# Optimization experiments

Hardware: AMD Instinct MI355X
Metric: run time of the kernel (lower is better)

## Reference

```python
import jax, jax.numpy as jnp
import numpy as np

DIM = 1024
HEADS = 16
HEAD_DIM = DIM // HEADS
SCALE = DIM ** (-0.5)  # note: module scales by full dim, not head_dim


def setup_inputs() -> dict:
    key = jax.random.key(0)
    k1, k2, k3, k4 = jax.random.split(key, 4)
    B, N = 4, 2048
    x = jax.random.normal(k1, (B, N, DIM), dtype=jnp.float32)
    # nn.Linear(dim, 3*dim, bias=False): weight [3*dim, dim]
    w_qkv = jax.random.normal(k2, (3 * DIM, DIM), dtype=jnp.float32) * (DIM ** -0.5)
    # nn.Linear(dim, dim) with bias
    w_out = jax.random.normal(k3, (DIM, DIM), dtype=jnp.float32) * (DIM ** -0.5)
    b_out = jax.random.normal(k4, (DIM,), dtype=jnp.float32) * 0.01
    return {"x": x, "w_qkv": w_qkv, "w_out": w_out, "b_out": b_out}


def reference(x, w_qkv, w_out, b_out):
    b, n, _ = x.shape
    qkv = jnp.einsum('bnd,ed->bne', x, w_qkv)  # [b, n, 3*dim]
    # rearrange 'b n (qkv h d) -> qkv b h n d'
    qkv = qkv.reshape(b, n, 3, HEADS, HEAD_DIM)
    q, k, v = (qkv[:, :, i].transpose(0, 2, 1, 3) for i in range(3))  # [b, h, n, d]
    dots = jnp.einsum('bhid,bhjd->bhij', q, k) * SCALE
    attn = jax.nn.softmax(dots, axis=-1)
    out = jnp.einsum('bhij,bhjd->bhid', attn, v)
    out = out.transpose(0, 2, 1, 3).reshape(b, n, HEADS * HEAD_DIM)  # [b, n, dim]
    return jnp.einsum('bnd,ed->bne', out, w_out) + b_out
```

## Files before the change

### kernel.cpp

```cpp
#include <hip/hip_runtime.h>

typedef __bf16 bf16_t;
typedef __bf16 bf16x2 __attribute__((ext_vector_type(2)));
typedef __bf16 bf16x4 __attribute__((ext_vector_type(4)));
typedef __bf16 bf16x8 __attribute__((ext_vector_type(8)));
typedef float floatx4 __attribute__((ext_vector_type(4)));

__device__ __forceinline__ void gll16(const void* g, void* l) {
  __builtin_amdgcn_global_load_lds(
      (const __attribute__((address_space(1))) void*)g,
      (__attribute__((address_space(3))) void*)l, 16, 0, 0);
}

__device__ __forceinline__ bf16x8 cvt8(const float4 a, const float4 b) {
  bf16x8 v;
  v[0] = (bf16_t)a.x; v[1] = (bf16_t)a.y; v[2] = (bf16_t)a.z; v[3] = (bf16_t)a.w;
  v[4] = (bf16_t)b.x; v[5] = (bf16_t)b.y; v[6] = (bf16_t)b.z; v[7] = (bf16_t)b.w;
  return v;
}

__global__ __launch_bounds__(256)
void cvt_f32_bf16(const float* __restrict__ src, bf16_t* __restrict__ dst, int n8)
{
  const int i = blockIdx.x * 256 + threadIdx.x;
  if (i < n8) {
    const float4 a = ((const float4*)src)[2 * i];
    const float4 b = ((const float4*)src)[2 * i + 1];
    *(bf16x8*)(dst + (size_t)i * 8) = cvt8(a, b);
  }
}

template<bool A32, bool W32, bool C32>
__global__ __launch_bounds__(256, 2)
void gemm_bt(const void* __restrict__ Av, const void* __restrict__ Wv,
             const float* __restrict__ bias, void* __restrict__ Cv,
             int M, int Nf, int K, int lda)
{
  __shared__ __align__(16) bf16_t lA[128 * 32];
  __shared__ __align__(16) bf16_t lB[128 * 32];

  const int tid  = threadIdx.x;
  const int wave = tid >> 6;
  const int lane = tid & 63;
  const int q    = lane >> 4;
  const int ln   = lane & 15;
  const int wm   = wave >> 1, wn = wave & 1;

  const int mtiles = M >> 7;
  const int mt = blockIdx.x % mtiles;
  const int nt = blockIdx.x / mtiles;
  const int m0 = mt << 7, n0 = nt << 7;

  floatx4 acc[4][4] = {};

  for (int k0 = 0; k0 < K; k0 += 32) {
    if constexpr (A32) {
      const float* Af = (const float*)Av;
#pragma unroll
      for (int sub = 0; sub < 2; ++sub) {
        const int r  = sub * 64 + (tid >> 2);
        const int c8 = tid & 3;
        const float* s = Af + (size_t)(m0 + r) * lda + k0 + c8 * 8;
        const float4 f0 = *(const float4*)s;
        const float4 f1 = *(const float4*)(s + 4);
        *(bf16x8*)(lA + r * 32 + (c8 ^ ((r >> 1) & 3)) * 8) = cvt8(f0, f1);
      }
    } else {
      const bf16_t* Ab = (const bf16_t*)Av;
#pragma unroll
      for (int half = 0; half < 2; ++half) {
        const int rbase = half * 64 + wave * 16;
        const int r  = rbase + (lane >> 2);
        const int gc = (lane & 3) ^ ((r >> 1) & 3);
        gll16(Ab + (size_t)(m0 + r) * lda + k0 + gc * 8, lA + rbase * 32);
      }
    }
    if constexpr (W32) {
      const float* Wf = (const float*)Wv;
#pragma unroll
      for (int sub = 0; sub < 2; ++sub) {
        const int r  = sub * 64 + (tid >> 2);
        const int c8 = tid & 3;
        const float* s = Wf + (size_t)(n0 + r) * K + k0 + c8 * 8;
        const float4 f0 = *(const float4*)s;
        const float4 f1 = *(const float4*)(s + 4);
        *(bf16x8*)(lB + r * 32 + (c8 ^ ((r >> 1) & 3)) * 8) = cvt8(f0, f1);
      }
    } else {
      const bf16_t* Wb = (const bf16_t*)Wv;
#pragma unroll
      for (int half = 0; half < 2; ++half) {
        const int rbase = half * 64 + wave * 16;
        const int r  = rbase + (lane >> 2);
        const int gc = (lane & 3) ^ ((r >> 1) & 3);
        gll16(Wb + (size_t)(n0 + r) * K + k0 + gc * 8, lB + rbase * 32);
      }
    }
    __syncthreads();

    bf16x8 af[4], bfr[4];
#pragma unroll
    for (int i = 0; i < 4; ++i) {
      const int r = wm * 64 + i * 16 + ln;
      af[i] = *(const bf16x8*)(lA + r * 32 + (q ^ ((r >> 1) & 3)) * 8);
    }
#pragma unroll
    for (int j = 0; j < 4; ++j) {
      const int r = wn * 64 + j * 16 + ln;
      bfr[j] = *(const bf16x8*)(lB + r * 32 + (q ^ ((r >> 1) & 3)) * 8);
    }
#pragma unroll
    for (int i = 0; i < 4; ++i)
#pragma unroll
      for (int j = 0; j < 4; ++j)
        acc[i][j] = __builtin_amdgcn_mfma_f32_16x16x32_bf16(af[i], bfr[j], acc[i][j], 0, 0, 0);
    __syncthreads();
  }

#pragma unroll
  for (int j = 0; j < 4; ++j) {
    const int col = n0 + wn * 64 + j * 16 + ln;
    const float bv = bias ? bias[col] : 0.0f;
#pragma unroll
    for (int i = 0; i < 4; ++i) {
      const int row = m0 + wm * 64 + i * 16 + q * 4;
#pragma unroll
      for (int r = 0; r < 4; ++r) {
        const float val = acc[i][j][r] + bv;
        if constexpr (C32)
          ((float*)Cv)[(size_t)(row + r) * Nf + col] = val;
        else
          ((bf16_t*)Cv)[(size_t)(row + r) * Nf + col] = (bf16_t)val;
      }
    }
  }
}

__global__ __launch_bounds__(256, 2)
void attn_kernel(bf16_t* __restrict__ qkv)
{
  __shared__ __align__(16) bf16_t lK[128 * 64];
  __shared__ __align__(16) bf16_t lV[128 * 66];
  __shared__ __align__(16) bf16_t lP[128 * 132];

  const int tid  = threadIdx.x;
  const int wave = tid >> 6;
  const int lane = tid & 63;
  const int q  = lane >> 4;
  const int ln = lane & 15;
  const int wm = wave >> 1, wn = wave & 1;

  const int bx = blockIdx.x;
  const int qt = bx & 15;
  const int h  = (bx >> 4) & 15;
  const int b  = bx >> 8;

  bf16_t* Qbase = qkv + (size_t)(b * 2048 + qt * 128) * 3072 + h * 64;
  const bf16_t* Kbase = qkv + (size_t)(b * 2048) * 3072 + 1024 + h * 64;
  const bf16_t* Vbase = qkv + (size_t)(b * 2048) * 3072 + 2048 + h * 64;

#pragma unroll
  for (int t = 0; t < 4; ++t) {
    const int rbase = t * 32 + wave * 8;
    const int r  = rbase + (lane >> 3);
    const int gc = (lane & 7) ^ (r & 7);
    gll16(Qbase + (size_t)r * 3072 + gc * 8, lP + rbase * 64);
  }
  __syncthreads();

  bf16x8 qf[4][2];
#pragma unroll
  for (int i = 0; i < 4; ++i) {
    const int r = wm * 64 + i * 16 + ln;
#pragma unroll
    for (int kt = 0; kt < 2; ++kt) {
      const int c = (kt * 4 + q) ^ (r & 7);
      qf[i][kt] = *(const bf16x8*)(lP + r * 64 + c * 8);
    }
  }
  __syncthreads();

  floatx4 accO[4][2] = {};
  floatx4 accS[4] = {};

  bf16x8 ones;
#pragma unroll
  for (int j = 0; j < 8; ++j) ones[j] = (bf16_t)1.0f;

  for (int jt = 0; jt < 16; ++jt) {
    const int j0 = jt * 128;

#pragma unroll
    for (int t = 0; t < 4; ++t) {
      const int rbase = t * 32 + wave * 8;
      const int r  = rbase + (lane >> 3);
      const int gc = (lane & 7) ^ (r & 7);
      gll16(Kbase + (size_t)(j0 + r) * 3072 + gc * 8, lK + rbase * 64);
    }

    {
      const int r = tid >> 1;
      const int hh = tid & 1;
      const bf16_t* src = Vbase + (size_t)(j0 + r) * 3072 + hh * 32;
#pragma unroll
      for (int k = 0; k < 4; ++k) {
        const bf16x8 v = *(const bf16x8*)(src + k * 8);
#pragma unroll
        for (int m = 0; m < 4; ++m) {
          bf16x2 pr;
          pr[0] = v[2 * m];
          pr[1] = v[2 * m + 1];
          *(bf16x2*)(lV + r * 66 + hh * 32 + k * 8 + 2 * m) = pr;
        }
      }
    }
    __syncthreads();

    bf16x8 kf[4][2];
#pragma unroll
    for (int n = 0; n < 4; ++n) {
      const int r = wn * 64 + n * 16 + ln;
#pragma unroll
      for (int kt = 0; kt < 2; ++kt) {
        const int c = (kt * 4 + q) ^ (r & 7);
        kf[n][kt] = *(const bf16x8*)(lK + r * 64 + c * 8);
      }
    }
#pragma unroll
    for (int i = 0; i < 4; ++i) {
      floatx4 s[4];
#pragma unroll
      for (int n = 0; n < 4; ++n) {
        floatx4 a = {0.0f, 0.0f, 0.0f, 0.0f};
        a = __builtin_amdgcn_mfma_f32_16x16x32_bf16(qf[i][0], kf[n][0], a, 0, 0, 0);
        a = __builtin_amdgcn_mfma_f32_16x16x32_bf16(qf[i][1], kf[n][1], a, 0, 0, 0);
        s[n] = a;
      }
#pragma unroll
      for (int r = 0; r < 4; ++r) {
        const int row = wm * 64 + i * 16 + q * 4 + r;
#pragma unroll
        for (int n = 0; n < 4; ++n) {
          const float e = __builtin_amdgcn_exp2f(s[n][r] * 0.04508422f);
          const int col = wn * 64 + n * 16 + ln;
          lP[row * 132 + col] = (bf16_t)e;
        }
      }
    }
    __syncthreads();

#pragma unroll
    for (int ks = 0; ks < 4; ++ks) {
      bf16x8 bv[2];
#pragma unroll
      for (int n = 0; n < 2; ++n) {
        const int d = wn * 32 + n * 16 + ln;
#pragma unroll
        for (int j = 0; j < 8; ++j) {
          const int tok = ks * 32 + q * 8 + j;
          bv[n][j] = lV[tok * 66 + d];
        }
      }
#pragma unroll
      for (int i = 0; i < 4; ++i) {
        const int m = wm * 64 + i * 16 + ln;
        const bf16x4 lo4 = *(const bf16x4*)(lP + m * 132 + ks * 32 + q * 8);
        const bf16x4 hi4 = *(const bf16x4*)(lP + m * 132 + ks * 32 + q * 8 + 4);
        bf16x8 ap;
        ap[0] = lo4[0]; ap[1] = lo4[1]; ap[2] = lo4[2]; ap[3] = lo4[3];
        ap[4] = hi4[0]; ap[5] = hi4[1]; ap[6] = hi4[2]; ap[7] = hi4[3];
        accO[i][0] = __builtin_amdgcn_mfma_f32_16x16x32_bf16(ap, bv[0], accO[i][0], 0, 0, 0);
        accO[i][1] = __builtin_amdgcn_mfma_f32_16x16x32_bf16(ap, bv[1], accO[i][1], 0, 0, 0);
        accS[i]    = __builtin_amdgcn_mfma_f32_16x16x32_bf16(ap, ones,  accS[i],    0, 0, 0);
      }
    }
    __syncthreads();
  }

#pragma unroll
  for (int i = 0; i < 4; ++i) {
#pragma unroll
    for (int r = 0; r < 4; ++r) {
      const int row = wm * 64 + i * 16 + q * 4 + r;
      const float rcp = 1.0f / fmaxf(accS[i][r], 1e-20f);
#pragma unroll
      for (int n = 0; n < 2; ++n) {
        const int col = wn * 32 + n * 16 + ln;
        Qbase[(size_t)row * 3072 + col] = (bf16_t)(accO[i][n][r] * rcp);
      }
    }
  }
}

extern "C" void kernel_launch(void* const* d_in, const int* in_sizes, int n_in,
                              void* d_out, int out_size, void* d_ws, size_t ws_size,
                              hipStream_t stream)
{
  const float* x     = (const float*)d_in[0];
  const float* w_qkv = (const float*)d_in[1];
  const float* w_out = (const float*)d_in[2];
  const float* b_out = (const float*)d_in[3];
  float* out = (float*)d_out;

  bf16_t* qkv    = (bf16_t*)d_ws;
  bf16_t* xb     = qkv    + (size_t)8192 * 3072;
  bf16_t* wqkvb  = xb     + (size_t)8192 * 1024;
  bf16_t* woutb  = wqkvb  + (size_t)3072 * 1024;

  cvt_f32_bf16<<<dim3(4096), dim3(256), 0, stream>>>(x,     xb,    8192 * 1024 / 8);
  cvt_f32_bf16<<<dim3(1536), dim3(256), 0, stream>>>(w_qkv, wqkvb, 3072 * 1024 / 8);
  cvt_f32_bf16<<<dim3(512),  dim3(256), 0, stream>>>(w_out, woutb, 1024 * 1024 / 8);

  gemm_bt<false, false, false><<<dim3(64 * 24), dim3(256), 0, stream>>>(
      xb, wqkvb, nullptr, qkv, 8192, 3072, 1024, 1024);
  attn_kernel<<<dim3(1024), dim3(256), 0, stream>>>(qkv);
  gemm_bt<false, false, true><<<dim3(64 * 8), dim3(256), 0, stream>>>(
      qkv, woutb, b_out, out, 8192, 1024, 1024, 3072);
}
```

Before: 322.4 us.

## Transpose V in LDS with swizzle and compute S^T for vectorized P stores

```diff
diff --git a/kernel.cpp b/kernel.cpp
--- a/kernel.cpp
+++ b/kernel.cpp
@@ -140,8 +140,8 @@
 void attn_kernel(bf16_t* __restrict__ qkv)
 {
   __shared__ __align__(16) bf16_t lK[128 * 64];
-  __shared__ __align__(16) bf16_t lV[128 * 66];
-  __shared__ __align__(16) bf16_t lP[128 * 132];
+  __shared__ __align__(16) bf16_t lVT[64 * 128];
+  __shared__ __align__(16) bf16_t lP[128 * 136];
 
   const int tid  = threadIdx.x;
   const int wave = tid >> 6;
@@ -199,18 +199,21 @@
     }
 
     {
-      const int r = tid >> 1;
-      const int hh = tid & 1;
-      const bf16_t* src = Vbase + (size_t)(j0 + r) * 3072 + hh * 32;
-#pragma unroll
-      for (int k = 0; k < 4; ++k) {
-        const bf16x8 v = *(const bf16x8*)(src + k * 8);
-#pragma unroll
-        for (int m = 0; m < 4; ++m) {
+      const int p = lane;
+#pragma unroll
+      for (int it = 0; it < 2; ++it) {
+        const int c = wave + it * 4;
+        const bf16_t* src = Vbase + (size_t)(j0 + 2 * p) * 3072 + c * 8;
+        const bf16x8 v0 = *(const bf16x8*)(src);
+        const bf16x8 v1 = *(const bf16x8*)(src + 3072);
+#pragma unroll
+        for (int j = 0; j < 8; ++j) {
+          const int d  = c * 8 + j;
+          const int ch = (p >> 2) ^ (d & 7);
           bf16x2 pr;
-          pr[0] = v[2 * m];
-          pr[1] = v[2 * m + 1];
-          *(bf16x2*)(lV + r * 66 + hh * 32 + k * 8 + 2 * m) = pr;
+          pr[0] = v0[j];
+          pr[1] = v1[j];
+          *(bf16x2*)(lVT + d * 128 + ch * 8 + ((2 * p) & 7)) = pr;
         }
       }
     }
@@ -228,23 +231,18 @@
     }
 #pragma unroll
     for (int i = 0; i < 4; ++i) {
-      floatx4 s[4];
 #pragma unroll
       for (int n = 0; n < 4; ++n) {
-        floatx4 a = {0.0f, 0.0f, 0.0f, 0.0f};
-        a = __builtin_amdgcn_mfma_f32_16x16x32_bf16(qf[i][0], kf[n][0], a, 0, 0, 0);
-        a = __builtin_amdgcn_mfma_f32_16x16x32_bf16(qf[i][1], kf[n][1], a, 0, 0, 0);
-        s[n] = a;
-      }
-#pragma unroll
-      for (int r = 0; r < 4; ++r) {
-        const int row = wm * 64 + i * 16 + q * 4 + r;
-#pragma unroll
-        for (int n = 0; n < 4; ++n) {
-          const float e = __builtin_amdgcn_exp2f(s[n][r] * 0.04508422f);
-          const int col = wn * 64 + n * 16 + ln;
-          lP[row * 132 + col] = (bf16_t)e;
-        }
+        floatx4 st = {0.0f, 0.0f, 0.0f, 0.0f};
+        st = __builtin_amdgcn_mfma_f32_16x16x32_bf16(kf[i][0], qf[n][0], st, 0, 0, 0);
+        st = __builtin_amdgcn_mfma_f32_16x16x32_bf16(kf[i][1], qf[n][1], st, 0, 0, 0);
+        bf16x4 pk;
+#pragma unroll
+        for (int r = 0; r < 4; ++r)
+          pk[r] = (bf16_t)__builtin_amdgcn_exp2f(st[r] * 0.04508422f);
+        const int m    = wm * 64 + n * 16 + ln;
+        const int tok0 = wn * 64 + i * 16 + q * 4;
+        *(bf16x4*)(lP + m * 136 + tok0) = pk;
       }
     }
     __syncthreads();
@@ -254,21 +252,14 @@
       bf16x8 bv[2];
 #pragma unroll
       for (int n = 0; n < 2; ++n) {
-        const int d = wn * 32 + n * 16 + ln;
-#pragma unroll
-        for (int j = 0; j < 8; ++j) {
-          const int tok = ks * 32 + q * 8 + j;
-          bv[n][j] = lV[tok * 66 + d];
-        }
+        const int d  = wn * 32 + n * 16 + ln;
+        const int cc = (ks * 4 + q) ^ (d & 7);
+        bv[n] = *(const bf16x8*)(lVT + d * 128 + cc * 8);
       }
 #pragma unroll
       for (int i = 0; i < 4; ++i) {
         const int m = wm * 64 + i * 16 + ln;
-        const bf16x4 lo4 = *(const bf16x4*)(lP + m * 132 + ks * 32 + q * 8);
-        const bf16x4 hi4 = *(const bf16x4*)(lP + m * 132 + ks * 32 + q * 8 + 4);
-        bf16x8 ap;
-        ap[0] = lo4[0]; ap[1] = lo4[1]; ap[2] = lo4[2]; ap[3] = lo4[3];
-        ap[4] = hi4[0]; ap[5] = hi4[1]; ap[6] = hi4[2]; ap[7] = hi4[3];
+        const bf16x8 ap = *(const bf16x8*)(lP + m * 136 + ks * 32 + q * 8);
         accO[i][0] = __builtin_amdgcn_mfma_f32_16x16x32_bf16(ap, bv[0], accO[i][0], 0, 0, 0);
         accO[i][1] = __builtin_amdgcn_mfma_f32_16x16x32_bf16(ap, bv[1], accO[i][1], 0, 0, 0);
         accS[i]    = __builtin_amdgcn_mfma_f32_16x16x32_bf16(ap, ones,  accS[i],    0, 0, 0);
```

Result: faster. 294.9 us (-8.5%).
